# Kernel optimization log

Hardware: AMD Instinct MI355X
Metric: run time of the kernel (lower is better)

Reference implementation:

```python
import jax, jax.numpy as jnp
import numpy as np

K = 16          # top-k from __init__ default
CHUNK = 64      # row chunk for memory-efficient L1 cdist (N % CHUNK == 0)


def cdist_l1(A, B):
    """Pairwise L1 distances [N, M] without materializing [N, M, D] at once."""
    N, D = A.shape
    A_chunks = A.reshape(N // CHUNK, CHUNK, D)
    def body(carry, a):  # a: [CHUNK, D]
        d = jnp.sum(jnp.abs(a[:, None, :] - B[None, :, :]), axis=-1)  # [CHUNK, M]
        return carry, d
    _, dists = jax.lax.scan(body, None, A_chunks)
    return dists.reshape(N, B.shape[0])


def setup_inputs() -> dict:
    key = jax.random.key(0)
    k1, k2, k3, k4 = jax.random.split(key, 4)
    N, D, L = 4096, 512, 128
    return {
        "gt_vals": jax.random.normal(k1, (N, D), dtype=jnp.float32),
        "train_latent": jax.random.normal(k2, (N, L), dtype=jnp.float32),
        "test_latent": jax.random.normal(k3, (N, L), dtype=jnp.float32),
        "W": jax.random.normal(k4, (L, D), dtype=jnp.float32) * (1.0 / np.sqrt(L)),
        "b": jnp.zeros((D,), dtype=jnp.float32),
    }


def reference(gt_vals, train_latent, test_latent, W, b):
    # decoder = linear; train samples are detached in the original module
    recovered_train = jax.lax.stop_gradient(train_latent @ W + b)  # [N, D]
    recovered_test = test_latent @ W + b                            # [N, D]

    positive_score_mat = 1.0 / cdist_l1(recovered_test, gt_vals)          # [N, N]
    negative_score_mat = 1.0 / cdist_l1(recovered_test, recovered_train)  # [N, N]

    positive_scores = jax.lax.top_k(positive_score_mat, K)[0].mean(-1)  # [N]
    negative_scores = jax.lax.top_k(negative_score_mat, K)[0].mean(-1)  # [N]

    losses = jax.nn.relu(negative_scores - positive_scores)
    # HuberLoss(delta=1.0) against zeros, mean reduction
    huber = jnp.where(losses <= 1.0, 0.5 * losses * losses, losses - 0.5)
    return huber.mean()
```

## Files before the change

### kernel.cpp

```cpp
#include <hip/hip_runtime.h>
#include <math.h>

#define N 4096
#define D 512
#define L 128

#define NP8 (D / 4)
#define BI 64
#define BJ 256

#define PARTS 16
#define PARTJ (N / PARTS)
#define TI 128
#define TJ 64
#define KD 32
#define AS_STRIDE (TI + 4)
#define BS_STRIDE (TJ + 4)
#define DS_STRIDE (TJ + 4)
#define SMEM_FLOATS (TI * DS_STRIDE)

__device__ __forceinline__ unsigned sad8(unsigned a, unsigned b, unsigned c) {
#if __has_builtin(__builtin_amdgcn_sad_u8)
  return __builtin_amdgcn_sad_u8(a, b, c);
#else
  unsigned d;
  asm("v_sad_u8 %0, %1, %2, %3" : "=v"(d) : "v"(a), "v"(b), "v"(c));
  return d;
#endif
}

__device__ __forceinline__ unsigned pack4(float4 v) {
  int q0 = min(max(__float2int_rn(v.x * 16.0f), -128), 127) + 128;
  int q1 = min(max(__float2int_rn(v.y * 16.0f), -128), 127) + 128;
  int q2 = min(max(__float2int_rn(v.z * 16.0f), -128), 127) + 128;
  int q3 = min(max(__float2int_rn(v.w * 16.0f), -128), 127) + 128;
  return (unsigned)q0 | ((unsigned)q1 << 8) | ((unsigned)q2 << 16) |
         ((unsigned)q3 << 24);
}

__device__ __forceinline__ void topk_insert(float (&tk)[16], float v) {
  float x = v;
#pragma unroll
  for (int k = 0; k < 16; ++k) {
    float lo = fminf(x, tk[k]);
    float hi = fmaxf(x, tk[k]);
    tk[k] = lo;
    x = hi;
  }
}

__device__ __forceinline__ void topk_insert_u32(unsigned (&tk)[16], unsigned v) {
  unsigned x = v;
#pragma unroll
  for (int k = 0; k < 16; ++k) {
    unsigned lo = tk[k] < x ? tk[k] : x;
    unsigned hi = tk[k] < x ? x : tk[k];
    tk[k] = lo;
    x = hi;
  }
}

__global__ __launch_bounds__(256) void linear_kernel(
    const float* __restrict__ lat_test, const float* __restrict__ lat_train,
    const float* __restrict__ W, const float* __restrict__ bias,
    float* __restrict__ rec_test, float* __restrict__ rec_train) {
  const float* __restrict__ lat = blockIdx.y ? lat_train : lat_test;
  float* __restrict__ out = blockIdx.y ? rec_train : rec_test;
  const int r0 = blockIdx.x * 8;
  const int t = threadIdx.x;

  __shared__ float ls[8 * L];
  {
    float4 v = *(const float4*)(lat + (size_t)r0 * L + t * 4);
    *(float4*)&ls[t * 4] = v;
  }
  __syncthreads();

  float acc[8][2];
#pragma unroll
  for (int r = 0; r < 8; ++r) { acc[r][0] = 0.f; acc[r][1] = 0.f; }

#pragma unroll 4
  for (int l = 0; l < L; ++l) {
    float w0 = W[l * D + t];
    float w1 = W[l * D + t + 256];
#pragma unroll
    for (int r = 0; r < 8; ++r) {
      float x = ls[r * L + l];
      acc[r][0] = fmaf(x, w0, acc[r][0]);
      acc[r][1] = fmaf(x, w1, acc[r][1]);
    }
  }
  float b0 = bias[t], b1 = bias[t + 256];
#pragma unroll
  for (int r = 0; r < 8; ++r) {
    out[(size_t)(r0 + r) * D + t] = acc[r][0] + b0;
    out[(size_t)(r0 + r) * D + t + 256] = acc[r][1] + b1;
  }
}

#define PKR 64
__global__ __launch_bounds__(256) void pack_kernel(
    const float* __restrict__ gt, const float* __restrict__ rec_test,
    const float* __restrict__ rec_train, unsigned* __restrict__ Gq,
    unsigned* __restrict__ Aq, unsigned* __restrict__ Tq) {
  const int which = blockIdx.y;
  const float* __restrict__ src =
      which == 0 ? gt : (which == 1 ? rec_test : rec_train);
  unsigned* __restrict__ dst = which == 0 ? Gq : (which == 1 ? Aq : Tq);
  const int i0 = blockIdx.x * PKR;
  const int tid = threadIdx.x;

  __shared__ unsigned ls[PKR][NP8 + 1];

#pragma unroll 4
  for (int s = 0; s < 32; ++s) {
    int flat = tid + s * 256;
    int row = flat >> 7;
    int c4 = flat & 127;
    float4 v = *(const float4*)(src + (size_t)(i0 + row) * D + c4 * 4);
    ls[row][c4] = pack4(v);
  }
  __syncthreads();

#pragma unroll 4
  for (int s = 0; s < 32; ++s) {
    int flat = tid + s * 256;
    int pd = flat >> 6;
    int i = flat & 63;
    dst[(size_t)pd * N + i0 + i] = ls[i][pd];
  }
}

__global__ __launch_bounds__(256)
void dist_sad_kernel(const unsigned* __restrict__ Aq,
                     const unsigned* __restrict__ Gq,
                     const unsigned* __restrict__ Tq,
                     unsigned short* __restrict__ dist) {
  const int i0 = blockIdx.x * BI;
  const int j0 = blockIdx.y * BJ;
  const int mat = blockIdx.z;
  const unsigned* __restrict__ Bq = mat ? Tq : Gq;
  unsigned short* __restrict__ out = dist + (size_t)mat * N * N;

  const int wave = threadIdx.x >> 6;
  const int lane = threadIdx.x & 63;
  const int iw = __builtin_amdgcn_readfirstlane(i0 + wave * 16);

  const unsigned* __restrict__ ap = Aq + iw;
  const unsigned* __restrict__ bp = Bq + j0 + 4 * lane;

  unsigned acc[16][4];
#pragma unroll
  for (int r = 0; r < 16; ++r)
#pragma unroll
    for (int c = 0; c < 4; ++c) acc[r][c] = 0u;

  uint4 bcur = *(const uint4*)(bp);
  bp += N;

#pragma unroll 2
  for (int pd = 0; pd < NP8; ++pd) {
    uint4 a0 = *(const uint4*)(ap);
    uint4 a1 = *(const uint4*)(ap + 4);
    uint4 a2 = *(const uint4*)(ap + 8);
    uint4 a3 = *(const uint4*)(ap + 12);
    ap += N;
    uint4 bnext;
    if (pd + 1 < NP8) {
      bnext = *(const uint4*)(bp);
      bp += N;
    }
#define SADQ(q, base)                                       \
    acc[base + 0][0] = sad8(q.x, bcur.x, acc[base + 0][0]); \
    acc[base + 0][1] = sad8(q.x, bcur.y, acc[base + 0][1]); \
    acc[base + 0][2] = sad8(q.x, bcur.z, acc[base + 0][2]); \
    acc[base + 0][3] = sad8(q.x, bcur.w, acc[base + 0][3]); \
    acc[base + 1][0] = sad8(q.y, bcur.x, acc[base + 1][0]); \
    acc[base + 1][1] = sad8(q.y, bcur.y, acc[base + 1][1]); \
    acc[base + 1][2] = sad8(q.y, bcur.z, acc[base + 1][2]); \
    acc[base + 1][3] = sad8(q.y, bcur.w, acc[base + 1][3]); \
    acc[base + 2][0] = sad8(q.z, bcur.x, acc[base + 2][0]); \
    acc[base + 2][1] = sad8(q.z, bcur.y, acc[base + 2][1]); \
    acc[base + 2][2] = sad8(q.z, bcur.z, acc[base + 2][2]); \
    acc[base + 2][3] = sad8(q.z, bcur.w, acc[base + 2][3]); \
    acc[base + 3][0] = sad8(q.w, bcur.x, acc[base + 3][0]); \
    acc[base + 3][1] = sad8(q.w, bcur.y, acc[base + 3][1]); \
    acc[base + 3][2] = sad8(q.w, bcur.z, acc[base + 3][2]); \
    acc[base + 3][3] = sad8(q.w, bcur.w, acc[base + 3][3]);
    SADQ(a0, 0) SADQ(a1, 4) SADQ(a2, 8) SADQ(a3, 12)
#undef SADQ
    bcur = bnext;
  }

#pragma unroll
  for (int r = 0; r < 16; ++r) {
    unsigned p0 = (acc[r][0] > 65535u ? 65535u : acc[r][0]) |
                  ((acc[r][1] > 65535u ? 65535u : acc[r][1]) << 16);
    unsigned p1 = (acc[r][2] > 65535u ? 65535u : acc[r][2]) |
                  ((acc[r][3] > 65535u ? 65535u : acc[r][3]) << 16);
    *(uint2*)(out + (size_t)(iw + r) * N + j0 + 4 * lane) = make_uint2(p0, p1);
  }
}

__global__ __launch_bounds__(256) void row_topk16_kernel(
    const unsigned short* __restrict__ dist, float* __restrict__ scores) {
  const int wave = threadIdx.x >> 6;
  const int lane = threadIdx.x & 63;
  const int row = blockIdx.x * 4 + wave;
  const unsigned* __restrict__ p =
      (const unsigned*)(dist + (size_t)row * N);

  unsigned tk[16];
#pragma unroll
  for (int k = 0; k < 16; ++k) tk[k] = 0xFFFFFFFFu;

#pragma unroll 1
  for (int q = 0; q < 8; ++q) {
    uint4 v = *(const uint4*)(p + q * 256 + lane * 4);
    unsigned v0 = v.x & 0xFFFFu, v1 = v.x >> 16;
    unsigned v2 = v.y & 0xFFFFu, v3 = v.y >> 16;
    unsigned v4 = v.z & 0xFFFFu, v5 = v.z >> 16;
    unsigned v6 = v.w & 0xFFFFu, v7 = v.w >> 16;
    if (v0 < tk[15]) topk_insert_u32(tk, v0);
    if (v1 < tk[15]) topk_insert_u32(tk, v1);
    if (v2 < tk[15]) topk_insert_u32(tk, v2);
    if (v3 < tk[15]) topk_insert_u32(tk, v3);
    if (v4 < tk[15]) topk_insert_u32(tk, v4);
    if (v5 < tk[15]) topk_insert_u32(tk, v5);
    if (v6 < tk[15]) topk_insert_u32(tk, v6);
    if (v7 < tk[15]) topk_insert_u32(tk, v7);
  }

#pragma unroll
  for (int m = 1; m < 64; m <<= 1) {
    unsigned oth[16];
#pragma unroll
    for (int k = 0; k < 16; ++k)
      oth[k] = (unsigned)__shfl_xor((int)tk[k], m, 64);
    unsigned lo[16];
#pragma unroll
    for (int k = 0; k < 16; ++k)
      lo[k] = tk[k] < oth[15 - k] ? tk[k] : oth[15 - k];
#pragma unroll
    for (int dlt = 8; dlt >= 1; dlt >>= 1) {
#pragma unroll
      for (int i = 0; i < 16; ++i) {
        if ((i & dlt) == 0 && (i + dlt) < 16) {
          unsigned a = lo[i], b = lo[i + dlt];
          lo[i] = a < b ? a : b;
          lo[i + dlt] = a < b ? b : a;
        }
      }
    }
#pragma unroll
    for (int k = 0; k < 16; ++k) tk[k] = lo[k];
  }

  if (lane == 0) {
    float s = 0.f;
#pragma unroll
    for (int k = 0; k < 16; ++k) s += 16.0f / (float)tk[k];
    scores[row] = s * (1.0f / 16.0f);
  }
}

__global__ __launch_bounds__(256) void dist_topk_kernel(
    const float* __restrict__ Arec, const float* __restrict__ Bgt,
    const float* __restrict__ Btr, float* __restrict__ cand) {
  const int itile = blockIdx.x;
  const int part = blockIdx.y;
  const int mat = blockIdx.z;
  const float* __restrict__ B = mat ? Btr : Bgt;
  const int i0 = itile * TI;
  const int jbase = part * PARTJ;

  __shared__ float smem[SMEM_FLOATS];
  float* As = smem;
  float* Bs = smem + KD * AS_STRIDE;
  float* distS = smem;

  const int tid = threadIdx.x;
  const int tx = tid & 15;
  const int ty = tid >> 4;
  const int srow = tid >> 1;
  const int shalf = tid & 1;
  const int scol = shalf * 32;

  float tk[16];
#pragma unroll
  for (int k = 0; k < 16; ++k) tk[k] = 3.0e38f;

  for (int jc = 0; jc < PARTJ; jc += TJ) {
    float acc[8][4];
#pragma unroll
    for (int r = 0; r < 8; ++r)
#pragma unroll
      for (int c = 0; c < 4; ++c) acc[r][c] = 0.f;

    for (int d0 = 0; d0 < D; d0 += KD) {
      __syncthreads();
#pragma unroll
      for (int s = 0; s < 4; ++s) {
        int f4 = tid + s * 256;
        int r = f4 >> 3;
        int c4 = f4 & 7;
        float4 v = *(const float4*)(Arec + (size_t)(i0 + r) * D + d0 + c4 * 4);
        As[(4 * c4 + 0) * AS_STRIDE + r] = v.x;
        As[(4 * c4 + 1) * AS_STRIDE + r] = v.y;
        As[(4 * c4 + 2) * AS_STRIDE + r] = v.z;
        As[(4 * c4 + 3) * AS_STRIDE + r] = v.w;
      }
#pragma unroll
      for (int s = 0; s < 2; ++s) {
        int f4 = tid + s * 256;
        int r = f4 >> 3;
        int c4 = f4 & 7;
        float4 v = *(const float4*)(B + (size_t)(jbase + jc + r) * D + d0 + c4 * 4);
        Bs[(4 * c4 + 0) * BS_STRIDE + r] = v.x;
        Bs[(4 * c4 + 1) * BS_STRIDE + r] = v.y;
        Bs[(4 * c4 + 2) * BS_STRIDE + r] = v.z;
        Bs[(4 * c4 + 3) * BS_STRIDE + r] = v.w;
      }
      __syncthreads();

#pragma unroll
      for (int d = 0; d < KD; ++d) {
        float4 a0 = *(const float4*)&As[d * AS_STRIDE + 8 * ty];
        float4 a1 = *(const float4*)&As[d * AS_STRIDE + 8 * ty + 4];
        float4 bv4 = *(const float4*)&Bs[d * BS_STRIDE + 4 * tx];
        float av[8] = {a0.x, a0.y, a0.z, a0.w, a1.x, a1.y, a1.z, a1.w};
        float bv[4] = {bv4.x, bv4.y, bv4.z, bv4.w};
#pragma unroll
        for (int r = 0; r < 8; ++r)
#pragma unroll
          for (int c = 0; c < 4; ++c) acc[r][c] += __builtin_fabsf(av[r] - bv[c]);
      }
    }

    __syncthreads();
#pragma unroll
    for (int r = 0; r < 8; ++r)
      *(float4*)&distS[(8 * ty + r) * DS_STRIDE + 4 * tx] =
          make_float4(acc[r][0], acc[r][1], acc[r][2], acc[r][3]);
    __syncthreads();

#pragma unroll 1
    for (int j4 = 0; j4 < 8; ++j4) {
      float4 v = *(const float4*)&distS[srow * DS_STRIDE + scol + j4 * 4];
      if (v.x < tk[15]) topk_insert(tk, v.x);
      if (v.y < tk[15]) topk_insert(tk, v.y);
      if (v.z < tk[15]) topk_insert(tk, v.z);
      if (v.w < tk[15]) topk_insert(tk, v.w);
    }
  }

  __syncthreads();
  float* mergeS = smem;
#pragma unroll
  for (int k4 = 0; k4 < 4; ++k4)
    *(float4*)&mergeS[srow * 32 + shalf * 16 + k4 * 4] =
        make_float4(tk[k4 * 4], tk[k4 * 4 + 1], tk[k4 * 4 + 2], tk[k4 * 4 + 3]);
  __syncthreads();

  if (tid < TI) {
    const float* LA = &mergeS[tid * 32];
    const float* LB = LA + 16;
    const int row = i0 + tid;
    float* dst = cand + ((size_t)((mat * PARTS + part) * N) + row) * 16;
    int ia = 0, ib = 0;
#pragma unroll 1
    for (int k = 0; k < 16; ++k) {
      float a = LA[ia < 16 ? ia : 15];
      float b = LB[ib < 16 ? ib : 15];
      bool takeA = (ib >= 16) || (ia < 16 && a <= b);
      dst[k] = takeA ? a : b;
      ia += takeA ? 1 : 0;
      ib += takeA ? 0 : 1;
    }
  }
}

__global__ __launch_bounds__(256) void merge_kernel(
    const float* __restrict__ cand, float* __restrict__ scores) {
  const int gid = blockIdx.x * 256 + threadIdx.x;
  if (gid >= 2 * N) return;
  const int m = gid >> 12;
  const int row = gid & (N - 1);

  float tk[16];
#pragma unroll
  for (int k = 0; k < 16; ++k) tk[k] = 3.0e38f;

  for (int p = 0; p < PARTS; ++p) {
    const float* lp = cand + ((size_t)((m * PARTS + p) * N) + row) * 16;
#pragma unroll 1
    for (int k = 0; k < 16; ++k) {
      float v = lp[k];
      if (v >= tk[15]) break;
      topk_insert(tk, v);
    }
  }
  float s = 0.f;
#pragma unroll
  for (int k = 0; k < 16; ++k) s += 1.0f / tk[k];
  scores[(size_t)m * N + row] = s * (1.0f / 16.0f);
}

__global__ __launch_bounds__(256) void loss_kernel(
    const float* __restrict__ scores, float* __restrict__ out) {
  const int tid = threadIdx.x;
  float s = 0.f;
  for (int i = tid; i < N; i += 256) {
    float l = scores[N + i] - scores[i];
    l = fmaxf(l, 0.f);
    s += (l <= 1.f) ? 0.5f * l * l : (l - 0.5f);
  }
#pragma unroll
  for (int off = 32; off > 0; off >>= 1) s += __shfl_down(s, off, 64);
  __shared__ float ws[4];
  if ((tid & 63) == 0) ws[tid >> 6] = s;
  __syncthreads();
  if (tid == 0) {
    float t = ws[0] + ws[1] + ws[2] + ws[3];
    out[0] = t * (1.0f / (float)N);
  }
}

extern "C" void kernel_launch(void* const* d_in, const int* in_sizes, int n_in,
                              void* d_out, int out_size, void* d_ws, size_t ws_size,
                              hipStream_t stream) {
  const float* gt_vals = (const float*)d_in[0];
  const float* train_latent = (const float*)d_in[1];
  const float* test_latent = (const float*)d_in[2];
  const float* W = (const float*)d_in[3];
  const float* b = (const float*)d_in[4];
  float* out = (float*)d_out;

  char* ws = (char*)d_ws;
  const size_t MB = 1048576;
  const size_t REC = 8 * MB;
  const size_t NEED_FAST = 90 * MB;

  if (ws_size >= NEED_FAST) {
    unsigned* Aq = (unsigned*)(ws);
    unsigned* Tq = (unsigned*)(ws + 2 * MB);
    unsigned* Gq = (unsigned*)(ws + 4 * MB);
    float* scores = (float*)(ws + 6 * MB);
    float* rec_test = (float*)(ws + 8 * MB);
    float* rec_train = (float*)(ws + 16 * MB);
    unsigned short* dist16 = (unsigned short*)(ws + 24 * MB);

    linear_kernel<<<dim3(N / 8, 2), 256, 0, stream>>>(
        test_latent, train_latent, W, b, rec_test, rec_train);
    pack_kernel<<<dim3(N / PKR, 3), 256, 0, stream>>>(
        gt_vals, rec_test, rec_train, Gq, Aq, Tq);
    dist_sad_kernel<<<dim3(N / BI, N / BJ, 2), 256, 0, stream>>>(
        Aq, Gq, Tq, dist16);
    row_topk16_kernel<<<(2 * N) / 4, 256, 0, stream>>>(dist16, scores);
    loss_kernel<<<1, 256, 0, stream>>>(scores, out);
  } else {
    float* rec_test = (float*)(ws);
    float* rec_train = (float*)(ws + REC);
    float* cand = (float*)(ws + 2 * REC);
    float* scores = (float*)(ws + 2 * REC + 8388608);
    linear_kernel<<<dim3(N / 8, 2), 256, 0, stream>>>(
        test_latent, train_latent, W, b, rec_test, rec_train);
    dist_topk_kernel<<<dim3(N / TI, PARTS, 2), 256, 0, stream>>>(
        rec_test, gt_vals, rec_train, cand);
    merge_kernel<<<(2 * N) / 256, 256, 0, stream>>>(cand, scores);
    loss_kernel<<<1, 256, 0, stream>>>(scores, out);
  }
}
```

Before: 279.4 us.

## Fuse linear decoder and int8 packing into one prep kernel; prefetch A in SAD loop

Replaces the separate linear and pack kernels with a single prep kernel that computes the decoder output in registers, quantizes it to 8 bits, and packs four values per word using cross-lane shuffles before writing the transposed layout. This removes the intermediate float rec_test and rec_train buffers, along with their global write and re-read and one kernel launch. The SAD distance loop also double-buffers the A operand loads so the next iteration's loads are issued before the current SAD work. The packed stores now go through strided 4-byte writes from one lane in four, which may coalesce less well than the old shared-memory transpose, and the extra prefetch registers raise register pressure in the SAD kernel.

```diff
diff --git a/kernel.cpp b/kernel.cpp
--- a/kernel.cpp
+++ b/kernel.cpp
@@ -29,13 +29,10 @@
 #endif
 }
 
-__device__ __forceinline__ unsigned pack4(float4 v) {
-  int q0 = min(max(__float2int_rn(v.x * 16.0f), -128), 127) + 128;
-  int q1 = min(max(__float2int_rn(v.y * 16.0f), -128), 127) + 128;
-  int q2 = min(max(__float2int_rn(v.z * 16.0f), -128), 127) + 128;
-  int q3 = min(max(__float2int_rn(v.w * 16.0f), -128), 127) + 128;
-  return (unsigned)q0 | ((unsigned)q1 << 8) | ((unsigned)q2 << 16) |
-         ((unsigned)q3 << 24);
+__device__ __forceinline__ unsigned q8(float x) {
+  int q = __float2int_rn(x * 16.0f);
+  q = min(max(q, -128), 127) + 128;
+  return (unsigned)q;
 }
 
 __device__ __forceinline__ void topk_insert(float (&tk)[16], float v) {
@@ -60,75 +57,67 @@
   }
 }
 
-__global__ __launch_bounds__(256) void linear_kernel(
-    const float* __restrict__ lat_test, const float* __restrict__ lat_train,
-    const float* __restrict__ W, const float* __restrict__ bias,
-    float* __restrict__ rec_test, float* __restrict__ rec_train) {
-  const float* __restrict__ lat = blockIdx.y ? lat_train : lat_test;
-  float* __restrict__ out = blockIdx.y ? rec_train : rec_test;
+__global__ __launch_bounds__(256) void prep_kernel(
+    const float* __restrict__ gt, const float* __restrict__ lat_test,
+    const float* __restrict__ lat_train, const float* __restrict__ W,
+    const float* __restrict__ bias, unsigned* __restrict__ Gq,
+    unsigned* __restrict__ Aq, unsigned* __restrict__ Tq) {
+  const int which = blockIdx.y;
+  unsigned* __restrict__ dst = which == 0 ? Gq : (which == 1 ? Aq : Tq);
   const int r0 = blockIdx.x * 8;
   const int t = threadIdx.x;
-
-  __shared__ float ls[8 * L];
-  {
-    float4 v = *(const float4*)(lat + (size_t)r0 * L + t * 4);
-    *(float4*)&ls[t * 4] = v;
-  }
-  __syncthreads();
-
-  float acc[8][2];
-#pragma unroll
-  for (int r = 0; r < 8; ++r) { acc[r][0] = 0.f; acc[r][1] = 0.f; }
+  const int lane = t & 63;
+
+  float vals[8][2];
+
+  if (which == 0) {
+#pragma unroll
+    for (int r = 0; r < 8; ++r) {
+      vals[r][0] = gt[(size_t)(r0 + r) * D + t];
+      vals[r][1] = gt[(size_t)(r0 + r) * D + t + 256];
+    }
+  } else {
+    const float* __restrict__ lat = (which == 1) ? lat_test : lat_train;
+    __shared__ float ls[8 * L];
+    {
+      float4 v = *(const float4*)(lat + (size_t)r0 * L + t * 4);
+      *(float4*)&ls[t * 4] = v;
+    }
+    __syncthreads();
+
+    float acc[8][2];
+#pragma unroll
+    for (int r = 0; r < 8; ++r) { acc[r][0] = 0.f; acc[r][1] = 0.f; }
 
 #pragma unroll 4
-  for (int l = 0; l < L; ++l) {
-    float w0 = W[l * D + t];
-    float w1 = W[l * D + t + 256];
+    for (int l = 0; l < L; ++l) {
+      float w0 = W[l * D + t];
+      float w1 = W[l * D + t + 256];
+#pragma unroll
+      for (int r = 0; r < 8; ++r) {
+        float x = ls[r * L + l];
+        acc[r][0] = fmaf(x, w0, acc[r][0]);
+        acc[r][1] = fmaf(x, w1, acc[r][1]);
+      }
+    }
+    float b0 = bias[t], b1 = bias[t + 256];
 #pragma unroll
     for (int r = 0; r < 8; ++r) {
-      float x = ls[r * L + l];
-      acc[r][0] = fmaf(x, w0, acc[r][0]);
-      acc[r][1] = fmaf(x, w1, acc[r][1]);
-    }
-  }
-  float b0 = bias[t], b1 = bias[t + 256];
-#pragma unroll
-  for (int r = 0; r < 8; ++r) {
-    out[(size_t)(r0 + r) * D + t] = acc[r][0] + b0;
-    out[(size_t)(r0 + r) * D + t + 256] = acc[r][1] + b1;
-  }
-}
-
-#define PKR 64
-__global__ __launch_bounds__(256) void pack_kernel(
-    const float* __restrict__ gt, const float* __restrict__ rec_test,
-    const float* __restrict__ rec_train, unsigned* __restrict__ Gq,
-    unsigned* __restrict__ Aq, unsigned* __restrict__ Tq) {
-  const int which = blockIdx.y;
-  const float* __restrict__ src =
-      which == 0 ? gt : (which == 1 ? rec_test : rec_train);
-  unsigned* __restrict__ dst = which == 0 ? Gq : (which == 1 ? Aq : Tq);
-  const int i0 = blockIdx.x * PKR;
-  const int tid = threadIdx.x;
-
-  __shared__ unsigned ls[PKR][NP8 + 1];
-
-#pragma unroll 4
-  for (int s = 0; s < 32; ++s) {
-    int flat = tid + s * 256;
-    int row = flat >> 7;
-    int c4 = flat & 127;
-    float4 v = *(const float4*)(src + (size_t)(i0 + row) * D + c4 * 4);
-    ls[row][c4] = pack4(v);
-  }
-  __syncthreads();
-
-#pragma unroll 4
-  for (int s = 0; s < 32; ++s) {
-    int flat = tid + s * 256;
-    int pd = flat >> 6;
-    int i = flat & 63;
-    dst[(size_t)pd * N + i0 + i] = ls[i][pd];
+      vals[r][0] = acc[r][0] + b0;
+      vals[r][1] = acc[r][1] + b1;
+    }
+  }
+
+#pragma unroll
+  for (int h = 0; h < 2; ++h) {
+    const int pd = (t >> 2) + h * 64;
+#pragma unroll
+    for (int r = 0; r < 8; ++r) {
+      unsigned u = q8(vals[r][h]);
+      unsigned p2 = u | (((unsigned)__shfl_down((int)u, 1, 64)) << 8);
+      unsigned w4 = p2 | (((unsigned)__shfl_down((int)p2, 2, 64)) << 16);
+      if ((lane & 3) == 0) dst[(size_t)pd * N + r0 + r] = w4;
+    }
   }
 }
 
@@ -156,18 +145,23 @@
 #pragma unroll
     for (int c = 0; c < 4; ++c) acc[r][c] = 0u;
 
+  uint4 a0c = *(const uint4*)(ap);
+  uint4 a1c = *(const uint4*)(ap + 4);
+  uint4 a2c = *(const uint4*)(ap + 8);
+  uint4 a3c = *(const uint4*)(ap + 12);
+  ap += N;
   uint4 bcur = *(const uint4*)(bp);
   bp += N;
 
 #pragma unroll 2
   for (int pd = 0; pd < NP8; ++pd) {
-    uint4 a0 = *(const uint4*)(ap);
-    uint4 a1 = *(const uint4*)(ap + 4);
-    uint4 a2 = *(const uint4*)(ap + 8);
-    uint4 a3 = *(const uint4*)(ap + 12);
-    ap += N;
-    uint4 bnext;
+    uint4 a0n, a1n, a2n, a3n, bnext;
     if (pd + 1 < NP8) {
+      a0n = *(const uint4*)(ap);
+      a1n = *(const uint4*)(ap + 4);
+      a2n = *(const uint4*)(ap + 8);
+      a3n = *(const uint4*)(ap + 12);
+      ap += N;
       bnext = *(const uint4*)(bp);
       bp += N;
     }
@@ -188,8 +182,9 @@
     acc[base + 3][1] = sad8(q.w, bcur.y, acc[base + 3][1]); \
     acc[base + 3][2] = sad8(q.w, bcur.z, acc[base + 3][2]); \
     acc[base + 3][3] = sad8(q.w, bcur.w, acc[base + 3][3]);
-    SADQ(a0, 0) SADQ(a1, 4) SADQ(a2, 8) SADQ(a3, 12)
+    SADQ(a0c, 0) SADQ(a1c, 4) SADQ(a2c, 8) SADQ(a3c, 12)
 #undef SADQ
+    a0c = a0n; a1c = a1n; a2c = a2n; a3c = a3n;
     bcur = bnext;
   }
 
@@ -265,6 +260,45 @@
   }
 }
 
+__global__ __launch_bounds__(256) void linear_kernel(
+    const float* __restrict__ lat_test, const float* __restrict__ lat_train,
+    const float* __restrict__ W, const float* __restrict__ bias,
+    float* __restrict__ rec_test, float* __restrict__ rec_train) {
+  const float* __restrict__ lat = blockIdx.y ? lat_train : lat_test;
+  float* __restrict__ out = blockIdx.y ? rec_train : rec_test;
+  const int r0 = blockIdx.x * 8;
+  const int t = threadIdx.x;
+
+  __shared__ float ls[8 * L];
+  {
+    float4 v = *(const float4*)(lat + (size_t)r0 * L + t * 4);
+    *(float4*)&ls[t * 4] = v;
+  }
+  __syncthreads();
+
+  float acc[8][2];
+#pragma unroll
+  for (int r = 0; r < 8; ++r) { acc[r][0] = 0.f; acc[r][1] = 0.f; }
+
+#pragma unroll 4
+  for (int l = 0; l < L; ++l) {
+    float w0 = W[l * D + t];
+    float w1 = W[l * D + t + 256];
+#pragma unroll
+    for (int r = 0; r < 8; ++r) {
+      float x = ls[r * L + l];
+      acc[r][0] = fmaf(x, w0, acc[r][0]);
+      acc[r][1] = fmaf(x, w1, acc[r][1]);
+    }
+  }
+  float b0 = bias[t], b1 = bias[t + 256];
+#pragma unroll
+  for (int r = 0; r < 8; ++r) {
+    out[(size_t)(r0 + r) * D + t] = acc[r][0] + b0;
+    out[(size_t)(r0 + r) * D + t + 256] = acc[r][1] + b1;
+  }
+}
+
 __global__ __launch_bounds__(256) void dist_topk_kernel(
     const float* __restrict__ Arec, const float* __restrict__ Bgt,
     const float* __restrict__ Btr, float* __restrict__ cand) {
@@ -440,21 +474,17 @@
   char* ws = (char*)d_ws;
   const size_t MB = 1048576;
   const size_t REC = 8 * MB;
-  const size_t NEED_FAST = 90 * MB;
+  const size_t NEED_FAST = 80 * MB;
 
   if (ws_size >= NEED_FAST) {
     unsigned* Aq = (unsigned*)(ws);
     unsigned* Tq = (unsigned*)(ws + 2 * MB);
     unsigned* Gq = (unsigned*)(ws + 4 * MB);
     float* scores = (float*)(ws + 6 * MB);
-    float* rec_test = (float*)(ws + 8 * MB);
-    float* rec_train = (float*)(ws + 16 * MB);
-    unsigned short* dist16 = (unsigned short*)(ws + 24 * MB);
-
-    linear_kernel<<<dim3(N / 8, 2), 256, 0, stream>>>(
-        test_latent, train_latent, W, b, rec_test, rec_train);
-    pack_kernel<<<dim3(N / PKR, 3), 256, 0, stream>>>(
-        gt_vals, rec_test, rec_train, Gq, Aq, Tq);
+    unsigned short* dist16 = (unsigned short*)(ws + 8 * MB);
+
+    prep_kernel<<<dim3(N / 8, 3), 256, 0, stream>>>(
+        gt_vals, test_latent, train_latent, W, b, Gq, Aq, Tq);
     dist_sad_kernel<<<dim3(N / BI, N / BJ, 2), 256, 0, stream>>>(
         Aq, Gq, Tq, dist16);
     row_topk16_kernel<<<(2 * N) / 4, 256, 0, stream>>>(dist16, scores);
```

Result: no change. 274.1 us (-1.9%).
